# Performance work log

Measured on AMD Instinct MI355X. Metric: run time of the kernel, lower is better.

## Reference

```python
import jax, jax.numpy as jnp
import numpy as np

B, T, H, NB, D, DH = 2, 8192, 16, 32, 1024, 128


def setup_inputs() -> dict:
    key = jax.random.key(0)
    ks = jax.random.split(key, 4)
    theta_path = jax.random.normal(ks[0], (B, T, H, NB), dtype=jnp.float32)
    content_emb = jax.random.normal(ks[1], (B, T, D), dtype=jnp.float32)
    W1 = jax.random.normal(ks[2], (D, DH), dtype=jnp.float32) / np.sqrt(D)
    b1 = jnp.zeros((DH,), dtype=jnp.float32)
    W2 = jax.random.normal(ks[3], (DH, H * NB), dtype=jnp.float32) / np.sqrt(DH)
    b2 = jnp.zeros((H * NB,), dtype=jnp.float32)
    log_Q = jnp.full((H, NB), -3.0, dtype=jnp.float32)  # torch init: full(-3.0)
    log_R = jnp.full((H, NB), 1.0, dtype=jnp.float32)   # torch init: full(1.0)
    return {"theta_path": theta_path, "content_emb": content_emb,
            "W1": W1, "b1": b1, "W2": W2, "b2": b2,
            "log_Q": log_Q, "log_R": log_R}


def _steady_state_K(log_Q, log_R):
    # closed-form scalar DARE: K* = (P+Q)/(P+Q+R), P = (-Q + sqrt(Q^2+4QR))/2
    Q = jnp.exp(log_Q)
    R = jnp.exp(log_R)
    P_post = 0.5 * (-Q + jnp.sqrt(Q * Q + 4.0 * Q * R))
    P_pred = P_post + Q
    return P_pred / (P_pred + R)


def _parallel_affine_scan(nu, K_star):
    # d_t = K * sum_{s<=t} (1-K)^(t-s) nu_s via zero-padded FFT convolution
    b, t, h, nb = nu.shape
    alpha = 1.0 - K_star                                   # (H, NB)
    k_idx = jnp.arange(t, dtype=nu.dtype)
    kernel = K_star[..., None] * (alpha[..., None] ** k_idx)  # (H, NB, T)
    pad_len = 2 * t
    kernel_fft = jnp.fft.rfft(kernel, n=pad_len, axis=-1)     # (H, NB, pad/2+1)
    nu_perm = jnp.transpose(nu, (0, 2, 3, 1))                 # (B, H, NB, T)
    nu_fft = jnp.fft.rfft(nu_perm, n=pad_len, axis=-1)
    conv = jnp.fft.irfft(nu_fft * kernel_fft[None], n=pad_len, axis=-1)[..., :t]
    return jnp.transpose(conv, (0, 3, 1, 2))                  # (B, T, H, NB)


def reference(theta_path, content_emb, W1, b1, W2, b2, log_Q, log_R):
    b, t, h, nb = theta_path.shape
    hid = jax.nn.gelu(content_emb @ W1 + b1, approximate=False)  # exact GELU (torch default)
    z_raw = (hid @ W2 + b2).reshape(b, t, h, nb)
    z = jnp.pi * jnp.tanh(z_raw)
    diff = z - theta_path
    nu = jnp.arctan2(jnp.sin(diff), jnp.cos(diff))  # wrap to (-pi, pi]
    K_star = _steady_state_K(log_Q, log_R)
    d = _parallel_affine_scan(nu, K_star)
    theta_hat = theta_path + d
    return theta_hat, d, K_star
```

## Files before the change

### kernel.cpp

```cpp
#include <hip/hip_runtime.h>
#include <math.h>

#define Bq 2
#define Tq 8192
#define Dq 1024
#define DHq 128
#define HNq 512
#define Mq (Bq*Tq)
#define NELEM ((size_t)Mq*HNq)
#define CHL 16
#define NCHK (Mq/CHL)
#define CH8 8
#define NC8 (Mq/CH8)
#define CPS8 (Tq/CH8)

typedef _Float16 half8 __attribute__((ext_vector_type(8)));
typedef float    f32x4 __attribute__((ext_vector_type(4)));

#define SC_LO  2048.0f
#define ISC_LO 4.8828125e-4f


__device__ __forceinline__ float gelu_exact(float x) {
    return 0.5f * x * (1.0f + erff(x * 0.7071067811865475f));
}

__device__ __forceinline__ float wrap_pi(float d) {
    return fmaf(-6.283185307179586f, rintf(d * 0.15915494309189535f), d);
}

__device__ __forceinline__ void gl16(const void* g, void* ldsDst) {
    __builtin_amdgcn_global_load_lds(
        (const __attribute__((address_space(1))) unsigned int*)g,
        (__attribute__((address_space(3))) unsigned int*)ldsDst, 16, 0, 0);
}

__global__ __launch_bounds__(64) void p0_pack(
    const float* __restrict__ W1, const float* __restrict__ W2,
    const float* __restrict__ lq, const float* __restrict__ lr,
    _Float16* __restrict__ w1h, _Float16* __restrict__ w1l,
    _Float16* __restrict__ w2h, _Float16* __restrict__ w2l,
    float* __restrict__ Karr, float* __restrict__ Aarr,
    float* __restrict__ kout)
{
    const int l = threadIdx.x;
    const int u = blockIdx.x;
    if (u == 384) {
        #pragma unroll
        for (int i = 0; i < 8; ++i) {
            int col = i * 64 + l;
            float Q = expf(lq[col]);
            float R = expf(lr[col]);
            float P = 0.5f * (-Q + sqrtf(fmaf(Q, Q, 4.0f * Q * R)));
            float Pp = P + Q;
            float K = Pp / (Pp + R);
            Karr[col] = K;
            Aarr[col] = 1.0f - K;
            kout[col] = K;
        }
        return;
    }
    const float* W; _Float16 *ph, *pl; int ncols, kt, ct, unit;
    if (u < 256) { unit = u;       kt = unit >> 3; ct = unit & 7;  W = W1; ph = w1h; pl = w1l; ncols = 128; }
    else         { unit = u - 256; kt = unit >> 5; ct = unit & 31; W = W2; ph = w2h; pl = w2l; ncols = 512; }
    const int col = ct * 16 + (l & 15);
    const int k0  = kt * 32 + ((l >> 4) * 8);
    half8 hv, lv;
    #pragma unroll
    for (int j = 0; j < 8; ++j) {
        float x = W[(size_t)(k0 + j) * ncols + col];
        _Float16 h = (_Float16)x;
        hv[j] = h;
        lv[j] = (_Float16)((x - (float)h) * SC_LO);
    }
    size_t off = ((size_t)unit * 64 + l) * 8;
    *(half8*)(ph + off) = hv;
    *(half8*)(pl + off) = lv;
}

__global__ __launch_bounds__(256, 1) void k1_mfma(
    const float* __restrict__ A, const _Float16* __restrict__ w1h,
    const _Float16* __restrict__ w1l, const float* __restrict__ b1,
    _Float16* __restrict__ hidH, _Float16* __restrict__ hidL)
{
    __shared__ char lds[131072];
    const int tid = threadIdx.x;
    const int w = tid >> 6, l = tid & 63;
    const int lrow = l & 15, lq = l >> 4;
    const int kh = w >> 1, ns = w & 1;
    const int rowb = blockIdx.x * 64;

    char* wbase = lds + w * 32768;
    const float* aLane = A + (size_t)(rowb + lrow) * Dq + kh * 512 + lq * 8;

#define STAGE(slot, s) do {                                                   \
        char* sb_ = wbase + (slot) * 16384;                                   \
        _Pragma("unroll")                                                     \
        for (int mi_ = 0; mi_ < 4; ++mi_) {                                   \
            _Pragma("unroll")                                                 \
            for (int hf_ = 0; hf_ < 2; ++hf_)                                 \
                gl16(aLane + (size_t)mi_ * 16 * Dq + (s) * 32 + hf_ * 4,      \
                     sb_ + (mi_ * 2 + hf_) * 1024);                           \
        }                                                                     \
        const int ktG_ = kh * 16 + (s);                                       \
        _Pragma("unroll")                                                     \
        for (int ct_ = 0; ct_ < 4; ++ct_) {                                   \
            size_t bo_ = ((size_t)(ktG_ * 8 + ns * 4 + ct_) * 64 + l) * 8;    \
            gl16(w1h + bo_, sb_ + 8192 + (ct_ * 2 + 0) * 1024);               \
            gl16(w1l + bo_, sb_ + 8192 + (ct_ * 2 + 1) * 1024);               \
        }                                                                     \
    } while (0)

    STAGE(0, 0);
    STAGE(1, 1);

    f32x4 accM[4][4] = {};
    f32x4 accC[4][4] = {};

    #pragma unroll 2
    for (int s = 0; s < 16; ++s) {
        asm volatile("s_waitcnt vmcnt(16)" ::: "memory");
        __builtin_amdgcn_sched_barrier(0);
        char* sb = wbase + (s & 1) * 16384;
        f32x4 av[4][2];
        half8 bh[4], bl[4];
        #pragma unroll
        for (int mi = 0; mi < 4; ++mi) {
            av[mi][0] = *(const f32x4*)(sb + (mi * 2 + 0) * 1024 + l * 16);
            av[mi][1] = *(const f32x4*)(sb + (mi * 2 + 1) * 1024 + l * 16);
        }
        #pragma unroll
        for (int ct = 0; ct < 4; ++ct) {
            bh[ct] = *(const half8*)(sb + 8192 + (ct * 2 + 0) * 1024 + l * 16);
            bl[ct] = *(const half8*)(sb + 8192 + (ct * 2 + 1) * 1024 + l * 16);
        }
        asm volatile("s_waitcnt lgkmcnt(0)" ::: "memory");
        __builtin_amdgcn_sched_barrier(0);
        int sp = s + 2; if (sp > 15) sp = 15;
        STAGE(s & 1, sp);

        #pragma unroll
        for (int mi = 0; mi < 4; ++mi) {
            half8 ah, alo;
            {
                float xs[8] = {av[mi][0][0], av[mi][0][1], av[mi][0][2], av[mi][0][3],
                               av[mi][1][0], av[mi][1][1], av[mi][1][2], av[mi][1][3]};
                #pragma unroll
                for (int j = 0; j < 8; ++j) {
                    _Float16 h = (_Float16)xs[j];
                    ah[j]  = h;
                    alo[j] = (_Float16)((xs[j] - (float)h) * SC_LO);
                }
            }
            #pragma unroll
            for (int ct = 0; ct < 4; ++ct) {
                accM[mi][ct] = __builtin_amdgcn_mfma_f32_16x16x32_f16(ah,  bh[ct], accM[mi][ct], 0, 0, 0);
                accC[mi][ct] = __builtin_amdgcn_mfma_f32_16x16x32_f16(ah,  bl[ct], accC[mi][ct], 0, 0, 0);
                accC[mi][ct] = __builtin_amdgcn_mfma_f32_16x16x32_f16(alo, bh[ct], accC[mi][ct], 0, 0, 0);
            }
        }
    }
#undef STAGE

    float* ldsR = (float*)lds;
    __syncthreads();
    if (kh == 0) {
        #pragma unroll
        for (int mi = 0; mi < 4; ++mi)
            #pragma unroll
            for (int ct = 0; ct < 4; ++ct) {
                const int ctG = ns * 4 + ct;
                #pragma unroll
                for (int r = 0; r < 4; ++r)
                    ldsR[(mi * 16 + lq * 4 + r) * 132 + ctG * 16 + lrow] =
                        fmaf(accC[mi][ct][r], ISC_LO, accM[mi][ct][r]);
            }
    }
    __syncthreads();
    if (kh == 1) {
        #pragma unroll
        for (int mi = 0; mi < 4; ++mi)
            #pragma unroll
            for (int ct = 0; ct < 4; ++ct) {
                const int ctG = ns * 4 + ct;
                #pragma unroll
                for (int r = 0; r < 4; ++r)
                    ldsR[(mi * 16 + lq * 4 + r) * 132 + ctG * 16 + lrow] +=
                        fmaf(accC[mi][ct][r], ISC_LO, accM[mi][ct][r]);
            }
    }
    __syncthreads();

    #pragma unroll
    for (int uh = 0; uh < 4; ++uh) {
        const int cl = w;
        const int kt = uh;
        const int dh0 = kt * 32 + lq * 8;
        const float* rp = ldsR + (cl * 16 + lrow) * 132 + dh0;
        f32x4 s0 = *(const f32x4*)rp;
        f32x4 s1 = *(const f32x4*)(rp + 4);
        f32x4 bb0 = *(const f32x4*)(b1 + dh0);
        f32x4 bb1 = *(const f32x4*)(b1 + dh0 + 4);
        half8 hv, lv;
        #pragma unroll
        for (int j = 0; j < 4; ++j) {
            float g = gelu_exact(s0[j] + bb0[j]);
            _Float16 h = (_Float16)g;
            hv[j] = h; lv[j] = (_Float16)((g - (float)h) * SC_LO);
        }
        #pragma unroll
        for (int j = 0; j < 4; ++j) {
            float g = gelu_exact(s1[j] + bb1[j]);
            _Float16 h = (_Float16)g;
            hv[4 + j] = h; lv[4 + j] = (_Float16)((g - (float)h) * SC_LO);
        }
        size_t off = (((size_t)(blockIdx.x * 4 + cl) * 4 + kt) * 64 + l) * 8;
        *(half8*)(hidH + off) = hv;
        *(half8*)(hidL + off) = lv;
    }
}

__global__ __launch_bounds__(256, 4) void k2a_mfma(
    const _Float16* __restrict__ hidH, const _Float16* __restrict__ hidL,
    const _Float16* __restrict__ w2h, const _Float16* __restrict__ w2l,
    const float* __restrict__ b2, const float* __restrict__ theta,
    const float* __restrict__ Karr, const float* __restrict__ Aarr,
    float* __restrict__ nuG, float* __restrict__ carries8)
{
    __shared__ float nuL[16][516];
    const int tid = threadIdx.x;
    const int w = tid >> 6, l = tid & 63;
    const int lrow = l & 15, lq = l >> 4;
    const int blk = blockIdx.x;

    f32x4 accM[8] = {};
    f32x4 accC[8] = {};
    #pragma unroll
    for (int kt = 0; kt < 4; ++kt) {
        size_t aoff = (((size_t)blk * 4 + kt) * 64 + l) * 8;
        const half8 ah  = *(const half8*)(hidH + aoff);
        const half8 alo = *(const half8*)(hidL + aoff);
        #pragma unroll
        for (int ct = 0; ct < 8; ++ct) {
            const int ctG = w * 8 + ct;
            size_t boff = (((size_t)kt * 32 + ctG) * 64 + l) * 8;
            const half8 bh = *(const half8*)(w2h + boff);
            const half8 bl = *(const half8*)(w2l + boff);
            accM[ct] = __builtin_amdgcn_mfma_f32_16x16x32_f16(ah,  bh, accM[ct], 0, 0, 0);
            accC[ct] = __builtin_amdgcn_mfma_f32_16x16x32_f16(ah,  bl, accC[ct], 0, 0, 0);
            accC[ct] = __builtin_amdgcn_mfma_f32_16x16x32_f16(alo, bh, accC[ct], 0, 0, 0);
        }
    }

    const float PI_F = 3.14159265358979323846f;
    #pragma unroll
    for (int ct = 0; ct < 8; ++ct) {
        const int col = w * 128 + ct * 16 + lrow;
        const float bb = b2[col];
        #pragma unroll
        for (int r = 0; r < 4; ++r) {
            const int row = blk * 16 + lq * 4 + r;
            float z = fmaf(accC[ct][r], ISC_LO, accM[ct][r]) + bb;
            float t = PI_F * tanhf(z);
            size_t io = (size_t)row * HNq + col;
            accM[ct][r] = wrap_pi(t - theta[io]);
        }
    }
    #pragma unroll
    for (int ct = 0; ct < 8; ++ct)
        #pragma unroll
        for (int r = 0; r < 4; ++r)
            nuL[lq * 4 + r][w * 128 + ct * 16 + lrow] = accM[ct][r];
    __syncthreads();

    #pragma unroll
    for (int cc = 0; cc < 2; ++cc) {
        const int col = tid + cc * 256;
        const float K = Karr[col], al = Aarr[col];
        #pragma unroll
        for (int sub = 0; sub < 2; ++sub) {
            float c = 0.0f;
            #pragma unroll
            for (int r = 0; r < 8; ++r)
                c = fmaf(al, c, K * nuL[sub * 8 + r][col]);
            carries8[(size_t)(blk * 2 + sub) * HNq + col] = c;
        }
    }
    f32x4* dst = (f32x4*)nuG + (size_t)blk * 2048;
    #pragma unroll
    for (int it = 0; it < 8; ++it) {
        const int g = tid + it * 256;
        const int row = g >> 7, cw = g & 127;
        dst[g] = *(const f32x4*)&nuL[row][cw * 4];
    }
}

__global__ __launch_bounds__(256) void k2b_scan(
    const float* __restrict__ theta, const float* __restrict__ Karr,
    const float* __restrict__ Aarr, const float* __restrict__ carries8,
    float* __restrict__ nud, float* __restrict__ theta_hat)
{
    const int tid = threadIdx.x;
    const int sub = tid >> 7, cg = tid & 127, c0 = cg * 4;
    const int chunk = blockIdx.x * 2 + sub;
    const int cloc = chunk & (CPS8 - 1);
    const int seq0 = chunk - cloc;

    const f32x4 K4 = *(const f32x4*)(Karr + c0);
    const f32x4 A4 = *(const f32x4*)(Aarr + c0);
    f32x4 A8;
    #pragma unroll
    for (int j = 0; j < 4; ++j) {
        float a2 = A4[j] * A4[j];
        float a4 = a2 * a2;
        A8[j] = a4 * a4;
    }
    float amax = fmaxf(fmaxf(A8[0], A8[1]), fmaxf(A8[2], A8[3]));
    int n = cloc;
    if (amax <= 0.0f) {
        n = 0;
    } else {
        float ln = logf(amax);
        if (ln < -1e-9f) {
            int nn = (int)ceilf(-34.0f / ln);
            if (nn < n) n = nn;
        }
    }
    f32x4 s = {0.0f, 0.0f, 0.0f, 0.0f};
    for (int j = cloc - n; j < cloc; ++j) {
        f32x4 cv = *(const f32x4*)(carries8 + (size_t)(seq0 + j) * HNq + c0);
        s = A8 * s + cv;
    }

    const size_t base = (size_t)chunk * CH8 * HNq + c0;
    #pragma unroll
    for (int r = 0; r < CH8; ++r) {
        const size_t idx = base + (size_t)r * HNq;
        f32x4 nu = *(const f32x4*)(nud + idx);
        f32x4 th = *(const f32x4*)(theta + idx);
        s = A4 * s + K4 * nu;
        *(f32x4*)(nud + idx) = s;
        *(f32x4*)(theta_hat + idx) = th + s;
    }
}

extern "C" void kernel_launch(void* const* d_in, const int* in_sizes, int n_in,
                              void* d_out, int out_size, void* d_ws, size_t ws_size,
                              hipStream_t stream) {
    const float* theta   = (const float*)d_in[0];
    const float* content = (const float*)d_in[1];
    const float* W1      = (const float*)d_in[2];
    const float* b1      = (const float*)d_in[3];
    const float* W2      = (const float*)d_in[4];
    const float* b2      = (const float*)d_in[5];
    const float* logQ    = (const float*)d_in[6];
    const float* logR    = (const float*)d_in[7];

    float* out       = (float*)d_out;
    float* theta_hat = out;
    float* dbuf      = out + NELEM;
    float* kout      = out + 2 * NELEM;

    _Float16* w1h  = (_Float16*)d_ws;
    _Float16* w1l  = w1h + 131072;
    _Float16* w2h  = w1l + 131072;
    _Float16* w2l  = w2h + 65536;
    _Float16* hidH = w2l + 65536;
    _Float16* hidL = hidH + 2097152;
    float* Karr    = (float*)(hidL + 2097152);
    float* Aarr    = Karr + 512;
    float* carries8 = Aarr + 512;

    p0_pack<<<dim3(385), 64, 0, stream>>>(W1, W2, logQ, logR,
                                          w1h, w1l, w2h, w2l, Karr, Aarr, kout);
    k1_mfma<<<dim3(Mq / 64), 256, 0, stream>>>(content, w1h, w1l, b1, hidH, hidL);
    k2a_mfma<<<dim3(NCHK), 256, 0, stream>>>(hidH, hidL, w2h, w2l, b2, theta,
                                             Karr, Aarr, dbuf, carries8);
    k2b_scan<<<dim3(NC8 / 2), 256, 0, stream>>>(theta, Karr, Aarr, carries8,
                                                dbuf, theta_hat);
}
```

Baseline: 212.2 us.

## Retile first GEMM with shared LDS staging across 8 waves and 32-row blocks

The first GEMM kernel changes from 4 waves each staging its own private A/B tiles to 8 waves per 32-row block that cooperatively load shared A and B tiles into a swizzled, double-buffered LDS, with workgroup barriers between stages. This removes duplicated global loads and cuts LDS per block so two blocks can fit per CU, at the cost of extra barriers and smaller per-wave MFMA work. The second kernel also batches its W2 fragment loads in groups of four and prefetches all theta values before the tanh/wrap epilogue, so memory latency can overlap the MFMAs.

```diff
diff --git a/kernel.cpp b/kernel.cpp
--- a/kernel.cpp
+++ b/kernel.cpp
@@ -78,73 +78,82 @@
     *(half8*)(pl + off) = lv;
 }
 
-__global__ __launch_bounds__(256, 1) void k1_mfma(
+__global__ __launch_bounds__(512, 2) void k1_mfma(
     const float* __restrict__ A, const _Float16* __restrict__ w1h,
     const _Float16* __restrict__ w1l, const float* __restrict__ b1,
     _Float16* __restrict__ hidH, _Float16* __restrict__ hidL)
 {
-    __shared__ char lds[131072];
+    __shared__ char lds[81920];
     const int tid = threadIdx.x;
     const int w = tid >> 6, l = tid & 63;
     const int lrow = l & 15, lq = l >> 4;
-    const int kh = w >> 1, ns = w & 1;
-    const int rowb = blockIdx.x * 64;
-
-    char* wbase = lds + w * 32768;
-    const float* aLane = A + (size_t)(rowb + lrow) * Dq + kh * 512 + lq * 8;
-
-#define STAGE(slot, s) do {                                                   \
-        char* sb_ = wbase + (slot) * 16384;                                   \
+    const int kh = w >> 2, ns = (w >> 1) & 1, ch = w & 1;
+    const int rowb = blockIdx.x * 32;
+
+    const int ar  = (w & 3) * 8 + (l >> 3);
+    const int ac4 = (l & 7) ^ (ar & 7);
+    const float* aSrc = A + (size_t)(rowb + ar) * Dq + (w >> 2) * 512 + ac4 * 4;
+    const _Float16* bS[4];
+    #pragma unroll
+    for (int i = 0; i < 4; ++i) {
+        const int r = w * 4 + i;
+        const int ctG = (r & 15) >> 1;
+        const _Float16* pl = (r & 1) ? w1l : w1h;
+        bS[i] = pl + (((size_t)(w >> 2) * 128 + ctG) * 64 + l) * 8;
+    }
+
+#define STAGE(slot, sL) do {                                                  \
+        gl16(aSrc + (sL) * 32, lds + (slot) * 8192 + w * 1024);               \
         _Pragma("unroll")                                                     \
-        for (int mi_ = 0; mi_ < 4; ++mi_) {                                   \
-            _Pragma("unroll")                                                 \
-            for (int hf_ = 0; hf_ < 2; ++hf_)                                 \
-                gl16(aLane + (size_t)mi_ * 16 * Dq + (s) * 32 + hf_ * 4,      \
-                     sb_ + (mi_ * 2 + hf_) * 1024);                           \
-        }                                                                     \
-        const int ktG_ = kh * 16 + (s);                                       \
-        _Pragma("unroll")                                                     \
-        for (int ct_ = 0; ct_ < 4; ++ct_) {                                   \
-            size_t bo_ = ((size_t)(ktG_ * 8 + ns * 4 + ct_) * 64 + l) * 8;    \
-            gl16(w1h + bo_, sb_ + 8192 + (ct_ * 2 + 0) * 1024);               \
-            gl16(w1l + bo_, sb_ + 8192 + (ct_ * 2 + 1) * 1024);               \
-        }                                                                     \
+        for (int i_ = 0; i_ < 4; ++i_)                                        \
+            gl16(bS[i_] + (size_t)(sL) * 4096,                                \
+                 lds + 16384 + (slot) * 32768 + (w * 4 + i_) * 1024);         \
     } while (0)
+
+    const int khA = kh * 4096, khB = kh * 16384;
+    const int aSw0 = ((lq * 2 + 0) ^ (lrow & 7)) * 16;
+    const int aSw1 = ((lq * 2 + 1) ^ (lrow & 7)) * 16;
+    const int sub0 = (ns * 4 + ch * 2 + 0) * 2;
+    const int sub1 = (ns * 4 + ch * 2 + 1) * 2;
 
     STAGE(0, 0);
     STAGE(1, 1);
 
-    f32x4 accM[4][4] = {};
-    f32x4 accC[4][4] = {};
+    f32x4 accM[2][2] = {};
+    f32x4 accC[2][2] = {};
 
     #pragma unroll 2
-    for (int s = 0; s < 16; ++s) {
-        asm volatile("s_waitcnt vmcnt(16)" ::: "memory");
+    for (int sL = 0; sL < 16; ++sL) {
+        asm volatile("s_waitcnt vmcnt(5)" ::: "memory");
         __builtin_amdgcn_sched_barrier(0);
-        char* sb = wbase + (s & 1) * 16384;
-        f32x4 av[4][2];
-        half8 bh[4], bl[4];
-        #pragma unroll
-        for (int mi = 0; mi < 4; ++mi) {
-            av[mi][0] = *(const f32x4*)(sb + (mi * 2 + 0) * 1024 + l * 16);
-            av[mi][1] = *(const f32x4*)(sb + (mi * 2 + 1) * 1024 + l * 16);
-        }
-        #pragma unroll
-        for (int ct = 0; ct < 4; ++ct) {
-            bh[ct] = *(const half8*)(sb + 8192 + (ct * 2 + 0) * 1024 + l * 16);
-            bl[ct] = *(const half8*)(sb + 8192 + (ct * 2 + 1) * 1024 + l * 16);
-        }
+        __builtin_amdgcn_s_barrier();
+        __builtin_amdgcn_sched_barrier(0);
+        char* As = lds + (sL & 1) * 8192;
+        char* Bs = lds + 16384 + (sL & 1) * 32768;
+        f32x4 a0[2], a1[2];
+        #pragma unroll
+        for (int mi = 0; mi < 2; ++mi) {
+            const int ro = khA + (mi * 16 + lrow) * 128;
+            a0[mi] = *(const f32x4*)(As + ro + aSw0);
+            a1[mi] = *(const f32x4*)(As + ro + aSw1);
+        }
+        half8 bh[2], bl[2];
+        bh[0] = *(const half8*)(Bs + khB + (sub0 + 0) * 1024 + l * 16);
+        bl[0] = *(const half8*)(Bs + khB + (sub0 + 1) * 1024 + l * 16);
+        bh[1] = *(const half8*)(Bs + khB + (sub1 + 0) * 1024 + l * 16);
+        bl[1] = *(const half8*)(Bs + khB + (sub1 + 1) * 1024 + l * 16);
         asm volatile("s_waitcnt lgkmcnt(0)" ::: "memory");
         __builtin_amdgcn_sched_barrier(0);
-        int sp = s + 2; if (sp > 15) sp = 15;
-        STAGE(s & 1, sp);
-
-        #pragma unroll
-        for (int mi = 0; mi < 4; ++mi) {
+        __builtin_amdgcn_s_barrier();
+        __builtin_amdgcn_sched_barrier(0);
+        { int sp = sL + 2; if (sp > 15) sp = 15; STAGE(sL & 1, sp); }
+
+        #pragma unroll
+        for (int mi = 0; mi < 2; ++mi) {
             half8 ah, alo;
             {
-                float xs[8] = {av[mi][0][0], av[mi][0][1], av[mi][0][2], av[mi][0][3],
-                               av[mi][1][0], av[mi][1][1], av[mi][1][2], av[mi][1][3]};
+                float xs[8] = {a0[mi][0], a0[mi][1], a0[mi][2], a0[mi][3],
+                               a1[mi][0], a1[mi][1], a1[mi][2], a1[mi][3]};
                 #pragma unroll
                 for (int j = 0; j < 8; ++j) {
                     _Float16 h = (_Float16)xs[j];
@@ -153,48 +162,48 @@
                 }
             }
             #pragma unroll
-            for (int ct = 0; ct < 4; ++ct) {
-                accM[mi][ct] = __builtin_amdgcn_mfma_f32_16x16x32_f16(ah,  bh[ct], accM[mi][ct], 0, 0, 0);
-                accC[mi][ct] = __builtin_amdgcn_mfma_f32_16x16x32_f16(ah,  bl[ct], accC[mi][ct], 0, 0, 0);
-                accC[mi][ct] = __builtin_amdgcn_mfma_f32_16x16x32_f16(alo, bh[ct], accC[mi][ct], 0, 0, 0);
+            for (int i = 0; i < 2; ++i) {
+                accM[mi][i] = __builtin_amdgcn_mfma_f32_16x16x32_f16(ah,  bh[i], accM[mi][i], 0, 0, 0);
+                accC[mi][i] = __builtin_amdgcn_mfma_f32_16x16x32_f16(ah,  bl[i], accC[mi][i], 0, 0, 0);
+                accC[mi][i] = __builtin_amdgcn_mfma_f32_16x16x32_f16(alo, bh[i], accC[mi][i], 0, 0, 0);
             }
         }
     }
 #undef STAGE
 
+    asm volatile("s_waitcnt vmcnt(0)" ::: "memory");
+    __syncthreads();
     float* ldsR = (float*)lds;
-    __syncthreads();
     if (kh == 0) {
         #pragma unroll
-        for (int mi = 0; mi < 4; ++mi)
-            #pragma unroll
-            for (int ct = 0; ct < 4; ++ct) {
-                const int ctG = ns * 4 + ct;
+        for (int mi = 0; mi < 2; ++mi)
+            #pragma unroll
+            for (int i = 0; i < 2; ++i) {
+                const int ctG = ns * 4 + ch * 2 + i;
                 #pragma unroll
                 for (int r = 0; r < 4; ++r)
                     ldsR[(mi * 16 + lq * 4 + r) * 132 + ctG * 16 + lrow] =
-                        fmaf(accC[mi][ct][r], ISC_LO, accM[mi][ct][r]);
+                        fmaf(accC[mi][i][r], ISC_LO, accM[mi][i][r]);
             }
     }
     __syncthreads();
     if (kh == 1) {
         #pragma unroll
-        for (int mi = 0; mi < 4; ++mi)
-            #pragma unroll
-            for (int ct = 0; ct < 4; ++ct) {
-                const int ctG = ns * 4 + ct;
+        for (int mi = 0; mi < 2; ++mi)
+            #pragma unroll
+            for (int i = 0; i < 2; ++i) {
+                const int ctG = ns * 4 + ch * 2 + i;
                 #pragma unroll
                 for (int r = 0; r < 4; ++r)
                     ldsR[(mi * 16 + lq * 4 + r) * 132 + ctG * 16 + lrow] +=
-                        fmaf(accC[mi][ct][r], ISC_LO, accM[mi][ct][r]);
+                        fmaf(accC[mi][i][r], ISC_LO, accM[mi][i][r]);
             }
     }
     __syncthreads();
 
-    #pragma unroll
-    for (int uh = 0; uh < 4; ++uh) {
-        const int cl = w;
-        const int kt = uh;
+    {
+        const int cl = w >> 2;
+        const int kt = w & 3;
         const int dh0 = kt * 32 + lq * 8;
         const float* rp = ldsR + (cl * 16 + lrow) * 132 + dh0;
         f32x4 s0 = *(const f32x4*)rp;
@@ -214,7 +223,7 @@
             _Float16 h = (_Float16)g;
             hv[4 + j] = h; lv[4 + j] = (_Float16)((g - (float)h) * SC_LO);
         }
-        size_t off = (((size_t)(blockIdx.x * 4 + cl) * 4 + kt) * 64 + l) * 8;
+        size_t off = (((size_t)(blockIdx.x * 2 + cl) * 4 + kt) * 64 + l) * 8;
         *(half8*)(hidH + off) = hv;
         *(half8*)(hidL + off) = lv;
     }
@@ -241,15 +250,32 @@
         const half8 ah  = *(const half8*)(hidH + aoff);
         const half8 alo = *(const half8*)(hidL + aoff);
         #pragma unroll
-        for (int ct = 0; ct < 8; ++ct) {
-            const int ctG = w * 8 + ct;
-            size_t boff = (((size_t)kt * 32 + ctG) * 64 + l) * 8;
-            const half8 bh = *(const half8*)(w2h + boff);
-            const half8 bl = *(const half8*)(w2l + boff);
-            accM[ct] = __builtin_amdgcn_mfma_f32_16x16x32_f16(ah,  bh, accM[ct], 0, 0, 0);
-            accC[ct] = __builtin_amdgcn_mfma_f32_16x16x32_f16(ah,  bl, accC[ct], 0, 0, 0);
-            accC[ct] = __builtin_amdgcn_mfma_f32_16x16x32_f16(alo, bh, accC[ct], 0, 0, 0);
-        }
+        for (int g = 0; g < 2; ++g) {
+            half8 bh[4], bl[4];
+            #pragma unroll
+            for (int i = 0; i < 4; ++i) {
+                const int ctG = w * 8 + g * 4 + i;
+                size_t boff = (((size_t)kt * 32 + ctG) * 64 + l) * 8;
+                bh[i] = *(const half8*)(w2h + boff);
+                bl[i] = *(const half8*)(w2l + boff);
+            }
+            #pragma unroll
+            for (int i = 0; i < 4; ++i) {
+                const int ct = g * 4 + i;
+                accM[ct] = __builtin_amdgcn_mfma_f32_16x16x32_f16(ah,  bh[i], accM[ct], 0, 0, 0);
+                accC[ct] = __builtin_amdgcn_mfma_f32_16x16x32_f16(ah,  bl[i], accC[ct], 0, 0, 0);
+                accC[ct] = __builtin_amdgcn_mfma_f32_16x16x32_f16(alo, bh[i], accC[ct], 0, 0, 0);
+            }
+        }
+    }
+
+    float th[8][4];
+    #pragma unroll
+    for (int ct = 0; ct < 8; ++ct) {
+        const int col = w * 128 + ct * 16 + lrow;
+        #pragma unroll
+        for (int r = 0; r < 4; ++r)
+            th[ct][r] = theta[(size_t)(blk * 16 + lq * 4 + r) * HNq + col];
     }
 
     const float PI_F = 3.14159265358979323846f;
@@ -259,11 +285,9 @@
         const float bb = b2[col];
         #pragma unroll
         for (int r = 0; r < 4; ++r) {
-            const int row = blk * 16 + lq * 4 + r;
             float z = fmaf(accC[ct][r], ISC_LO, accM[ct][r]) + bb;
             float t = PI_F * tanhf(z);
-            size_t io = (size_t)row * HNq + col;
-            accM[ct][r] = wrap_pi(t - theta[io]);
+            accM[ct][r] = wrap_pi(t - th[ct][r]);
         }
     }
     #pragma unroll
@@ -373,7 +397,7 @@
 
     p0_pack<<<dim3(385), 64, 0, stream>>>(W1, W2, logQ, logR,
                                           w1h, w1l, w2h, w2l, Karr, Aarr, kout);
-    k1_mfma<<<dim3(Mq / 64), 256, 0, stream>>>(content, w1h, w1l, b1, hidH, hidL);
+    k1_mfma<<<dim3(Mq / 32), 512, 0, stream>>>(content, w1h, w1l, b1, hidH, hidL);
     k2a_mfma<<<dim3(NCHK), 256, 0, stream>>>(hidH, hidL, w2h, w2l, b2, theta,
                                              Karr, Aarr, dbuf, carries8);
     k2b_scan<<<dim3(NC8 / 2), 256, 0, stream>>>(theta, Karr, Aarr, carries8,
```

Result: no change. 209.8 us (-1.1%).
